# Optimization experiments

Hardware: AMD Instinct MI355X
Metric: run time of the kernel (lower is better)

## Reference

```python
import jax, jax.numpy as jnp
import numpy as np

H = 16          # heads_num
EPS_LN = 1e-6
EPS_RMS = 1e-6


def _layernorm(x):
    # elementwise_affine=False LayerNorm over last dim
    mu = jnp.mean(x, axis=-1, keepdims=True)
    var = jnp.mean(jnp.square(x - mu), axis=-1, keepdims=True)
    return (x - mu) * jax.lax.rsqrt(var + EPS_LN)


def _rmsnorm(x, w):
    # per-head RMSNorm over head_dim with affine weight
    ms = jnp.mean(jnp.square(x), axis=-1, keepdims=True)
    return x * jax.lax.rsqrt(ms + EPS_RMS) * w


def setup_inputs() -> dict:
    key = jax.random.key(0)
    ks = jax.random.split(key, 16)
    B, L, C = 2, 2048, 2048
    D = C // H
    Cm = 4 * C  # mlp hidden (mlp_width_ratio=4)
    s = 0.02
    return {
        "txt": jax.random.normal(ks[0], (B, L, C), jnp.float32),
        "vec_txt": jax.random.normal(ks[1], (B, C), jnp.float32),
        "mod_w": jax.random.normal(ks[2], (C, 6 * C), jnp.float32) * s,
        "mod_b": jnp.zeros((6 * C,), jnp.float32),
        "q_w": jax.random.normal(ks[3], (C, C), jnp.float32) * s,
        "k_w": jax.random.normal(ks[4], (C, C), jnp.float32) * s,
        "v_w": jax.random.normal(ks[5], (C, C), jnp.float32) * s,
        "qn_w": jnp.ones((D,), jnp.float32),
        "kn_w": jnp.ones((D,), jnp.float32),
        "proj_w": jax.random.normal(ks[6], (C, C), jnp.float32) * s,
        "fc1_w": jax.random.normal(ks[7], (C, Cm), jnp.float32) * s,
        "fc1_b": jnp.zeros((Cm,), jnp.float32),
        "fc2_w": jax.random.normal(ks[8], (Cm, C), jnp.float32) * s,
        "fc2_b": jnp.zeros((C,), jnp.float32),
    }


def _block(txt, vec_txt, mod_w, mod_b, q_w, k_w, v_w, qn_w, kn_w,
           proj_w, fc1_w, fc1_b, fc2_w, fc2_b):
    B, L, C = txt.shape
    D = C // H
    # ModulateDiT: Linear(silu(vec)) -> 6 chunks
    mod = jax.nn.silu(vec_txt) @ mod_w + mod_b                  # [B, 6C]
    sh1, sc1, g1, sh2, sc2, g2 = jnp.split(mod, 6, axis=-1)     # each [B, C]

    xm = _layernorm(txt) * (1.0 + sc1[:, None, :]) + sh1[:, None, :]
    q = (xm @ q_w).reshape(B, L, H, D)
    k = (xm @ k_w).reshape(B, L, H, D)
    v = (xm @ v_w).reshape(B, L, H, D)
    q = _rmsnorm(q, qn_w)
    k = _rmsnorm(k, kn_w)

    # causal scaled dot-product attention
    scores = jnp.einsum('blhd,bmhd->bhlm', q, k) / jnp.sqrt(jnp.float32(D))
    causal = jnp.tril(jnp.ones((L, L), bool))
    scores = jnp.where(causal[None, None], scores, jnp.finfo(scores.dtype).min)
    probs = jax.nn.softmax(scores, axis=-1)
    attn = jnp.einsum('bhlm,bmhd->blhd', probs, v).reshape(B, L, C)

    txt = txt + g1[:, None, :] * (attn @ proj_w)

    x2 = _layernorm(txt) * (1.0 + sc2[:, None, :]) + sh2[:, None, :]
    mlp = jax.nn.gelu(x2 @ fc1_w + fc1_b, approximate=True) @ fc2_w + fc2_b
    txt = txt + g2[:, None, :] * mlp
    return txt


def reference(txt, vec_txt, mod_w, mod_b, q_w, k_w, v_w, qn_w, kn_w,
              proj_w, fc1_w, fc1_b, fc2_w, fc2_b):
    return _block(txt, vec_txt, mod_w, mod_b, q_w, k_w, v_w, qn_w, kn_w,
                  proj_w, fc1_w, fc1_b, fc2_w, fc2_b)
```

## Files before the change

### kernel.cpp

```cpp
#include <hip/hip_runtime.h>
#include <math.h>

typedef unsigned short u16;
typedef unsigned int   u32;
typedef __attribute__((ext_vector_type(8))) short short8;
typedef __attribute__((ext_vector_type(4))) float f32x4;

#define H_   16
#define B_   2
#define L_   2048
#define C_   2048
#define D_   128
#define CM_  8192
#define SIXC_ (6*C_)
#define M_   (B_*L_)

__device__ __forceinline__ u16 f2bf(float f) {
  u32 u = __float_as_uint(f);
  u = (u + 0x7fffu + ((u >> 16) & 1u)) >> 16;
  return (u16)u;
}

__global__ __launch_bounds__(256)
void wt_transpose(const float* __restrict__ Wf, u16* __restrict__ Wt, int K, int N)
{
  __shared__ float tile[32][33];
  const int n0 = blockIdx.x * 32, k0 = blockIdx.y * 32;
  const int t = threadIdx.x;
  const int r = t >> 5, c = t & 31;
  #pragma unroll
  for (int i = 0; i < 4; i++)
    tile[i*8 + r][c] = Wf[(long)(k0 + i*8 + r)*N + n0 + c];
  __syncthreads();
  #pragma unroll
  for (int i = 0; i < 4; i++)
    Wt[(long)(n0 + i*8 + r)*K + k0 + c] = f2bf(tile[c][i*8 + r]);
}

__global__ __launch_bounds__(256)
void v_transpose(const float* __restrict__ vf, u16* __restrict__ vt)
{
  __shared__ float tile[32][33];
  const int l0 = blockIdx.x * 32, d0 = blockIdx.y * 32;
  const int bh = blockIdx.z;
  const int b = bh >> 4, h = bh & 15;
  const int t = threadIdx.x;
  const int r = t >> 5, c = t & 31;
  #pragma unroll
  for (int i = 0; i < 4; i++)
    tile[i*8 + r][c] = vf[(((long)b*L_ + l0 + i*8 + r)*H_ + h)*D_ + d0 + c];
  __syncthreads();
  #pragma unroll
  for (int i = 0; i < 4; i++)
    vt[((long)bh*D_ + d0 + i*8 + r)*L_ + l0 + c] = f2bf(tile[c][i*8 + r]);
}

__global__ __launch_bounds__(256)
void mod_init(const float* __restrict__ mb, float* __restrict__ mod)
{
  int i = blockIdx.x * 256 + threadIdx.x;
  mod[i] = mb[i % SIXC_];
}

__global__ __launch_bounds__(256)
void mod_accum(const float* __restrict__ vec, const float* __restrict__ mw,
               float* __restrict__ mod)
{
  const int j  = blockIdx.x * 256 + threadIdx.x;
  const int c0 = blockIdx.y * 128;
  const int b  = blockIdx.z;
  float s = 0.f;
  for (int c = c0; c < c0 + 128; c++) {
    float v  = vec[b*C_ + c];
    float sv = v / (1.0f + expf(-v));
    s += sv * mw[(long)c*SIXC_ + j];
  }
  atomicAdd(&mod[b*SIXC_ + j], s);
}

__global__ __launch_bounds__(256)
void ln_mod(const float* __restrict__ x, const float* __restrict__ mod,
            u16* __restrict__ out, int sh_off, int sc_off)
{
  const int row = blockIdx.x;
  const int b   = row >> 11;
  const int t   = threadIdx.x;
  const int l   = t & 63, w = t >> 6;
  const float* xr = x + (long)row * C_;
  float4 v0 = *(const float4*)(xr + t*8);
  float4 v1 = *(const float4*)(xr + t*8 + 4);
  float xs[8] = {v0.x, v0.y, v0.z, v0.w, v1.x, v1.y, v1.z, v1.w};
  float s = 0.f;
  #pragma unroll
  for (int i = 0; i < 8; i++) s += xs[i];
  #pragma unroll
  for (int o = 1; o < 64; o <<= 1) s += __shfl_xor(s, o, 64);
  __shared__ float r1[4], r2[4];
  if (l == 0) r1[w] = s;
  __syncthreads();
  float mu = (r1[0] + r1[1] + r1[2] + r1[3]) * (1.0f / C_);
  float vs = 0.f;
  #pragma unroll
  for (int i = 0; i < 8; i++) { float d = xs[i] - mu; vs += d*d; }
  #pragma unroll
  for (int o = 1; o < 64; o <<= 1) vs += __shfl_xor(vs, o, 64);
  if (l == 0) r2[w] = vs;
  __syncthreads();
  float var  = (r2[0] + r2[1] + r2[2] + r2[3]) * (1.0f / C_);
  float rstd = rsqrtf(var + 1e-6f);
  const float* shp = mod + b*SIXC_ + sh_off;
  const float* scp = mod + b*SIXC_ + sc_off;
  u16 o8[8];
  #pragma unroll
  for (int i = 0; i < 8; i++) {
    int col = t*8 + i;
    o8[i] = f2bf((xs[i] - mu)*rstd*(1.0f + scp[col]) + shp[col]);
  }
  *(short8*)(out + (long)row*C_ + t*8) = *(short8*)o8;
}

__global__ __launch_bounds__(256)
void rms_cast(const float* __restrict__ in, const float* __restrict__ w,
              u16* __restrict__ out)
{
  const int row = blockIdx.x;
  const int t   = threadIdx.x;
  const long base = (long)row*C_ + t*8;
  float4 v0 = *(const float4*)(in + base);
  float4 v1 = *(const float4*)(in + base + 4);
  float xs[8] = {v0.x, v0.y, v0.z, v0.w, v1.x, v1.y, v1.z, v1.w};
  float ss = 0.f;
  #pragma unroll
  for (int i = 0; i < 8; i++) ss += xs[i]*xs[i];
  #pragma unroll
  for (int o = 1; o < 16; o <<= 1) ss += __shfl_xor(ss, o, 64);
  float sc = rsqrtf(ss * (1.0f/D_) + 1e-6f);
  const int d0 = (t & 15) * 8;
  u16 o8[8];
  #pragma unroll
  for (int i = 0; i < 8; i++) o8[i] = f2bf(xs[i]*sc*w[d0 + i]);
  *(short8*)(out + base) = *(short8*)o8;
}

template<int MODE>
__global__ __launch_bounds__(256)
void gemm_bt(const u16* __restrict__ A, const u16* __restrict__ Bt,
             int N, int K,
             float* __restrict__ Cf, u16* __restrict__ Cb,
             const float* __restrict__ bias,
             const float* __restrict__ resid,
             const float* __restrict__ mod, int goff)
{
  __shared__ __attribute__((aligned(16))) u16 As[128*32];
  __shared__ __attribute__((aligned(16))) u16 Bs[128*32];
  const int tid = threadIdx.x;
  const int l   = tid & 63;
  const int llo = l & 15, lhi = l >> 4;
  const int w   = tid >> 6;
  const int m0 = blockIdx.y * 128, n0 = blockIdx.x * 128;
  const int wm = (w >> 1) * 64, wn = (w & 1) * 64;

  const u16* Ag = A  + (long)m0 * K;
  const u16* Bg = Bt + (long)n0 * K;

  const int srow0 = (w*2)*16 + (l >> 2);
  const int skoff = (l & 3) * 8;

  f32x4 acc[4][4];
  #pragma unroll
  for (int i = 0; i < 4; i++)
    #pragma unroll
    for (int j = 0; j < 4; j++) acc[i][j] = (f32x4){0.f, 0.f, 0.f, 0.f};

  for (int k0 = 0; k0 < K; k0 += 32) {
    __syncthreads();
    #pragma unroll
    for (int i = 0; i < 2; i++) {
      const u16* ga = Ag + (long)(srow0 + i*16)*K + k0 + skoff;
      const u16* gb = Bg + (long)(srow0 + i*16)*K + k0 + skoff;
      __builtin_amdgcn_global_load_lds(
          (const __attribute__((address_space(1))) void*)ga,
          (__attribute__((address_space(3))) void*)(As + (w*2 + i)*512), 16, 0, 0);
      __builtin_amdgcn_global_load_lds(
          (const __attribute__((address_space(1))) void*)gb,
          (__attribute__((address_space(3))) void*)(Bs + (w*2 + i)*512), 16, 0, 0);
    }
    __syncthreads();
    short8 a[4], b[4];
    #pragma unroll
    for (int f = 0; f < 4; f++) {
      a[f] = *(const short8*)&As[(wm + f*16 + llo)*32 + lhi*8];
      b[f] = *(const short8*)&Bs[(wn + f*16 + llo)*32 + lhi*8];
    }
    #pragma unroll
    for (int mf = 0; mf < 4; mf++)
      #pragma unroll
      for (int nf = 0; nf < 4; nf++)
        acc[mf][nf] = __builtin_amdgcn_mfma_f32_16x16x32_bf16(a[mf], b[nf], acc[mf][nf], 0, 0, 0);
  }

  #pragma unroll
  for (int mf = 0; mf < 4; mf++) {
    #pragma unroll
    for (int j = 0; j < 4; j++) {
      const int  r  = m0 + wm + mf*16 + lhi*4 + j;
      const long rb = (long)r * N;
      const int  bb = r >> 11;
      #pragma unroll
      for (int nf = 0; nf < 4; nf++) {
        const int col = n0 + wn + nf*16 + llo;
        float x = acc[mf][nf][j];
        if (MODE == 0) {
          Cf[rb + col] = x;
        } else if (MODE == 1) {
          x += bias[col];
          float g = 0.5f*x*(1.0f + tanhf(0.7978845608028654f*(x + 0.044715f*x*x*x)));
          Cb[rb + col] = f2bf(g);
        } else if (MODE == 2) {
          Cf[rb + col] = resid[rb + col] + mod[bb*SIXC_ + goff + col] * x;
        } else {
          Cf[rb + col] = resid[rb + col] + mod[bb*SIXC_ + goff + col] * (x + bias[col]);
        }
      }
    }
  }
}

__global__ __launch_bounds__(256)
void attn(const u16* __restrict__ qb, const u16* __restrict__ kb,
          const u16* __restrict__ vt, u16* __restrict__ out)
{
  const int w = threadIdx.x >> 6;
  const int l = threadIdx.x & 63;
  const int p  = blockIdx.x * 4 + w;
  const int bh = blockIdx.y;
  const int b = bh >> 4, h = bh & 15;
  const int llo = l & 15, lhi = l >> 4;

  __shared__ __attribute__((aligned(16))) u16 Plds[4][16*32];
  u16* Pl = &Plds[w][0];

  const u16* kbase = kb + ((long)b*L_*H_ + h)*D_;
  const u16* vbase = vt + (long)bh*D_*L_;
  const float scale = 0.08838834764831845f;

  #pragma unroll
  for (int pass = 0; pass < 2; pass++) {
    const int qt = pass ? (127 - p) : p;
    const int q0 = qt * 16;

    short8 qf[4];
    const u16* qrow = qb + (((long)b*L_ + q0 + llo)*H_ + h)*D_;
    #pragma unroll
    for (int dc = 0; dc < 4; dc++) qf[dc] = *(const short8*)(qrow + dc*32 + lhi*8);

    f32x4 o[8];
    #pragma unroll
    for (int f = 0; f < 8; f++) o[f] = (f32x4){0.f, 0.f, 0.f, 0.f};
    float mreg = -1e30f, lsum = 0.f;

    const int ntiles = (q0 + 16 + 31) >> 5;

    for (int kt = 0; kt < ntiles; kt++) {
      const int kv0 = kt * 32;
      f32x4 st[2];
      st[0] = (f32x4){0.f,0.f,0.f,0.f};
      st[1] = (f32x4){0.f,0.f,0.f,0.f};
      #pragma unroll
      for (int mf = 0; mf < 2; mf++) {
        const u16* krow = kbase + (long)(kv0 + mf*16 + llo)*(H_*D_);
        #pragma unroll
        for (int dc = 0; dc < 4; dc++) {
          short8 kfr = *(const short8*)(krow + dc*32 + lhi*8);
          st[mf] = __builtin_amdgcn_mfma_f32_16x16x32_bf16(kfr, qf[dc], st[mf], 0, 0, 0);
        }
      }
      const int qcol = q0 + llo;
      float sv[8];
      float tmax = -1e30f;
      #pragma unroll
      for (int mf = 0; mf < 2; mf++)
        #pragma unroll
        for (int j = 0; j < 4; j++) {
          int key = kv0 + mf*16 + lhi*4 + j;
          float x = st[mf][j] * scale;
          x = (key > qcol) ? -1e30f : x;
          sv[mf*4 + j] = x;
          tmax = fmaxf(tmax, x);
        }
      tmax = fmaxf(tmax, __shfl_xor(tmax, 16, 64));
      tmax = fmaxf(tmax, __shfl_xor(tmax, 32, 64));
      float mnew  = fmaxf(mreg, tmax);
      float alpha = __expf(mreg - mnew);
      float psum = 0.f;
      u16 pb[8];
      #pragma unroll
      for (int i = 0; i < 8; i++) {
        float pp = __expf(sv[i] - mnew);
        psum += pp;
        pb[i] = f2bf(pp);
      }
      psum += __shfl_xor(psum, 16, 64);
      psum += __shfl_xor(psum, 32, 64);
      lsum = lsum*alpha + psum;
      mreg = mnew;
      #pragma unroll
      for (int j = 0; j < 4; j++) {
        float aj = __shfl(alpha, lhi*4 + j, 64);
        #pragma unroll
        for (int f = 0; f < 8; f++) o[f][j] *= aj;
      }
      #pragma unroll
      for (int mf = 0; mf < 2; mf++) {
        u32 w0 = (u32)pb[mf*4+0] | ((u32)pb[mf*4+1] << 16);
        u32 w1 = (u32)pb[mf*4+2] | ((u32)pb[mf*4+3] << 16);
        *(u32*)&Pl[llo*32 + mf*16 + lhi*4]     = w0;
        *(u32*)&Pl[llo*32 + mf*16 + lhi*4 + 2] = w1;
      }
      asm volatile("s_waitcnt lgkmcnt(0)" ::: "memory");
      short8 pf = *(const short8*)&Pl[llo*32 + lhi*8];
      #pragma unroll
      for (int f = 0; f < 8; f++) {
        short8 vfr = *(const short8*)(vbase + (long)(f*16 + llo)*L_ + kv0 + lhi*8);
        o[f] = __builtin_amdgcn_mfma_f32_16x16x32_bf16(pf, vfr, o[f], 0, 0, 0);
      }
      asm volatile("s_waitcnt lgkmcnt(0)" ::: "memory");
    }

    #pragma unroll
    for (int j = 0; j < 4; j++) {
      float lq  = __shfl(lsum, lhi*4 + j, 64);
      float inv = 1.0f / lq;
      const int qr = q0 + lhi*4 + j;
      u16* orow = out + ((long)b*L_ + qr)*C_ + h*D_;
      #pragma unroll
      for (int f = 0; f < 8; f++)
        orow[f*16 + llo] = f2bf(o[f][j] * inv);
    }
  }
}

extern "C" void kernel_launch(void* const* d_in, const int* in_sizes, int n_in,
                              void* d_out, int out_size, void* d_ws, size_t ws_size,
                              hipStream_t stream)
{
  const float* txt    = (const float*)d_in[0];
  const float* vec    = (const float*)d_in[1];
  const float* mod_w  = (const float*)d_in[2];
  const float* mod_b  = (const float*)d_in[3];
  const float* q_w    = (const float*)d_in[4];
  const float* k_w    = (const float*)d_in[5];
  const float* v_w    = (const float*)d_in[6];
  const float* qn_w   = (const float*)d_in[7];
  const float* kn_w   = (const float*)d_in[8];
  const float* proj_w = (const float*)d_in[9];
  const float* fc1_w  = (const float*)d_in[10];
  const float* fc1_b  = (const float*)d_in[11];
  const float* fc2_w  = (const float*)d_in[12];
  const float* fc2_b  = (const float*)d_in[13];
  float* out = (float*)d_out;

  char* ws = (char*)d_ws;
  size_t off = 0;
  auto alloc = [&](size_t bytes) {
    size_t r = off; off += (bytes + 255) & ~(size_t)255; return r;
  };
  float* mod  = (float*)(ws + alloc((size_t)B_*SIXC_*4));
  u16*  qwt   = (u16*)(ws + alloc((size_t)C_*C_*2));
  u16*  kwt   = (u16*)(ws + alloc((size_t)C_*C_*2));
  u16*  vwt   = (u16*)(ws + alloc((size_t)C_*C_*2));
  u16*  pwt   = (u16*)(ws + alloc((size_t)C_*C_*2));
  u16*  f1wt  = (u16*)(ws + alloc((size_t)C_*CM_*2));
  u16*  f2wt  = (u16*)(ws + alloc((size_t)C_*CM_*2));
  u16*  xm    = (u16*)(ws + alloc((size_t)M_*C_*2));
  float* qf   = (float*)(ws + alloc((size_t)M_*C_*4));
  float* kf   = (float*)(ws + alloc((size_t)M_*C_*4));
  float* vf   = (float*)(ws + alloc((size_t)M_*C_*4));
  u16*  qbb   = (u16*)(ws + alloc((size_t)M_*C_*2));
  u16*  kbb   = (u16*)(ws + alloc((size_t)M_*C_*2));
  u16*  vtt   = (u16*)(ws + alloc((size_t)M_*C_*2));
  u16*   h1     = (u16*)kf;
  float* txt2   = qf;
  u16*   x2m    = qbb;
  u16*   attn_o = xm;

  wt_transpose<<<dim3(C_/32,  C_/32 ), 256, 0, stream>>>(q_w,    qwt,  C_,  C_);
  wt_transpose<<<dim3(C_/32,  C_/32 ), 256, 0, stream>>>(k_w,    kwt,  C_,  C_);
  wt_transpose<<<dim3(C_/32,  C_/32 ), 256, 0, stream>>>(v_w,    vwt,  C_,  C_);
  wt_transpose<<<dim3(C_/32,  C_/32 ), 256, 0, stream>>>(proj_w, pwt,  C_,  C_);
  wt_transpose<<<dim3(CM_/32, C_/32 ), 256, 0, stream>>>(fc1_w,  f1wt, C_,  CM_);
  wt_transpose<<<dim3(C_/32,  CM_/32), 256, 0, stream>>>(fc2_w,  f2wt, CM_, C_);

  mod_init <<<dim3(B_*SIXC_/256), 256, 0, stream>>>(mod_b, mod);
  mod_accum<<<dim3(SIXC_/256, C_/128, B_), 256, 0, stream>>>(vec, mod_w, mod);

  ln_mod<<<dim3(M_), 256, 0, stream>>>(txt, mod, xm, 0, C_);

  gemm_bt<0><<<dim3(C_/128, M_/128), 256, 0, stream>>>(xm, qwt, C_, C_, qf, nullptr, nullptr, nullptr, nullptr, 0);
  gemm_bt<0><<<dim3(C_/128, M_/128), 256, 0, stream>>>(xm, kwt, C_, C_, kf, nullptr, nullptr, nullptr, nullptr, 0);
  gemm_bt<0><<<dim3(C_/128, M_/128), 256, 0, stream>>>(xm, vwt, C_, C_, vf, nullptr, nullptr, nullptr, nullptr, 0);

  rms_cast<<<dim3(M_), 256, 0, stream>>>(qf, qn_w, qbb);
  rms_cast<<<dim3(M_), 256, 0, stream>>>(kf, kn_w, kbb);
  v_transpose<<<dim3(L_/32, D_/32, B_*H_), 256, 0, stream>>>(vf, vtt);

  attn<<<dim3(L_/16/4/2, B_*H_), 256, 0, stream>>>(qbb, kbb, vtt, attn_o);

  gemm_bt<2><<<dim3(C_/128, M_/128), 256, 0, stream>>>(attn_o, pwt, C_, C_, txt2, nullptr, nullptr, txt, mod, 2*C_);

  ln_mod<<<dim3(M_), 256, 0, stream>>>(txt2, mod, x2m, 3*C_, 4*C_);

  gemm_bt<1><<<dim3(CM_/128, M_/128), 256, 0, stream>>>(x2m, f1wt, CM_, C_, nullptr, h1, fc1_b, nullptr, nullptr, 0);

  gemm_bt<3><<<dim3(C_/128, M_/128), 256, 0, stream>>>(h1, f2wt, C_, CM_, out, nullptr, fc2_b, txt2, mod, 5*C_);
}
```

Before: 1.322 ms.

## Pre-swizzle Q/K/V into MFMA fragment order and give each attention wave one tile

After: 1.251 ms. 1.06x faster.

```diff
diff --git a/kernel.cpp b/kernel.cpp
--- a/kernel.cpp
+++ b/kernel.cpp
@@ -38,7 +38,7 @@
 }
 
 __global__ __launch_bounds__(256)
-void v_transpose(const float* __restrict__ vf, u16* __restrict__ vt)
+void v_transpose(const float* __restrict__ vf, u16* __restrict__ vp)
 {
   __shared__ float tile[32][33];
   const int l0 = blockIdx.x * 32, d0 = blockIdx.y * 32;
@@ -50,9 +50,18 @@
   for (int i = 0; i < 4; i++)
     tile[i*8 + r][c] = vf[(((long)b*L_ + l0 + i*8 + r)*H_ + h)*D_ + d0 + c];
   __syncthreads();
-  #pragma unroll
-  for (int i = 0; i < 4; i++)
-    vt[((long)bh*D_ + d0 + i*8 + r)*L_ + l0 + c] = f2bf(tile[c][i*8 + r]);
+  if (t < 128) {
+    const int dl  = t >> 2;
+    const int oct = t & 3;
+    const int d   = d0 + dl;
+    const int f   = d >> 4, vllo = d & 15;
+    const int kt  = l0 >> 5;
+    u16 o8[8];
+    #pragma unroll
+    for (int e = 0; e < 8; e++) o8[e] = f2bf(tile[oct*8 + e][dl]);
+    u16* dst = vp + (((((long)bh*64 + kt)*8 + f)*4 + oct)*16 + vllo)*8;
+    *(short8*)dst = *(short8*)o8;
+  }
 }
 
 __global__ __launch_bounds__(256)
@@ -120,11 +129,15 @@
 }
 
 __global__ __launch_bounds__(256)
-void rms_cast(const float* __restrict__ in, const float* __restrict__ w,
-              u16* __restrict__ out)
+void rms_swz(const float* __restrict__ in, const float* __restrict__ w,
+             u16* __restrict__ out)
 {
   const int row = blockIdx.x;
+  const int b = row >> 11, lseq = row & 2047;
+  const int g = lseq >> 4, llo = lseq & 15;
   const int t   = threadIdx.x;
+  const int h   = t >> 4, c16 = t & 15;
+  const int dc  = c16 >> 2, lhi = c16 & 3;
   const long base = (long)row*C_ + t*8;
   float4 v0 = *(const float4*)(in + base);
   float4 v1 = *(const float4*)(in + base + 4);
@@ -135,11 +148,12 @@
   #pragma unroll
   for (int o = 1; o < 16; o <<= 1) ss += __shfl_xor(ss, o, 64);
   float sc = rsqrtf(ss * (1.0f/D_) + 1e-6f);
-  const int d0 = (t & 15) * 8;
+  const int d0 = c16 * 8;
   u16 o8[8];
   #pragma unroll
   for (int i = 0; i < 8; i++) o8[i] = f2bf(xs[i]*sc*w[d0 + i]);
-  *(short8*)(out + base) = *(short8*)o8;
+  u16* dst = out + (((((long)(b*H_ + h)*128 + g)*4 + dc)*4 + lhi)*16 + llo)*8;
+  *(short8*)dst = *(short8*)o8;
 }
 
 template<int MODE>
@@ -226,117 +240,119 @@
   }
 }
 
-__global__ __launch_bounds__(256)
-void attn(const u16* __restrict__ qb, const u16* __restrict__ kb,
-          const u16* __restrict__ vt, u16* __restrict__ out)
+__global__ __launch_bounds__(256, 4)
+void attn(const u16* __restrict__ qs, const u16* __restrict__ ks,
+          const u16* __restrict__ vp, u16* __restrict__ out)
 {
   const int w = threadIdx.x >> 6;
   const int l = threadIdx.x & 63;
-  const int p  = blockIdx.x * 4 + w;
+  const int qt = 127 - (blockIdx.x * 4 + w);
   const int bh = blockIdx.y;
-  const int b = bh >> 4, h = bh & 15;
+  const int b = bh >> 4;
+  const int h = bh & 15;
   const int llo = l & 15, lhi = l >> 4;
 
   __shared__ __attribute__((aligned(16))) u16 Plds[4][16*32];
   u16* Pl = &Plds[w][0];
 
-  const u16* kbase = kb + ((long)b*L_*H_ + h)*D_;
-  const u16* vbase = vt + (long)bh*D_*L_;
+  const u16* qbase = qs + ((long)bh*128 + qt)*2048;
+  const u16* kbase = ks + (long)bh*262144;
+  const u16* vbase = vp + (long)bh*262144;
   const float scale = 0.08838834764831845f;
 
-  #pragma unroll
-  for (int pass = 0; pass < 2; pass++) {
-    const int qt = pass ? (127 - p) : p;
-    const int q0 = qt * 16;
-
-    short8 qf[4];
-    const u16* qrow = qb + (((long)b*L_ + q0 + llo)*H_ + h)*D_;
-    #pragma unroll
-    for (int dc = 0; dc < 4; dc++) qf[dc] = *(const short8*)(qrow + dc*32 + lhi*8);
-
-    f32x4 o[8];
-    #pragma unroll
-    for (int f = 0; f < 8; f++) o[f] = (f32x4){0.f, 0.f, 0.f, 0.f};
-    float mreg = -1e30f, lsum = 0.f;
-
-    const int ntiles = (q0 + 16 + 31) >> 5;
-
-    for (int kt = 0; kt < ntiles; kt++) {
-      const int kv0 = kt * 32;
-      f32x4 st[2];
-      st[0] = (f32x4){0.f,0.f,0.f,0.f};
-      st[1] = (f32x4){0.f,0.f,0.f,0.f};
+  short8 qf[4];
+  #pragma unroll
+  for (int dc = 0; dc < 4; dc++)
+    qf[dc] = *(const short8*)(qbase + dc*512 + l*8);
+
+  f32x4 o[8];
+  #pragma unroll
+  for (int f = 0; f < 8; f++) o[f] = (f32x4){0.f, 0.f, 0.f, 0.f};
+  float mreg = -1e30f, lsum = 0.f;
+
+  const int ntiles = (qt + 2) >> 1;
+  const int qcol = qt*16 + llo;
+
+  for (int kt = 0; kt < ntiles; kt++) {
+    const int kv0 = kt * 32;
+    const u16* ktb = kbase + (long)kt*4096;
+    const u16* vtb = vbase + (long)kt*4096;
+
+    f32x4 st[2];
+    st[0] = (f32x4){0.f,0.f,0.f,0.f};
+    st[1] = (f32x4){0.f,0.f,0.f,0.f};
+    #pragma unroll
+    for (int mf = 0; mf < 2; mf++) {
       #pragma unroll
-      for (int mf = 0; mf < 2; mf++) {
-        const u16* krow = kbase + (long)(kv0 + mf*16 + llo)*(H_*D_);
-        #pragma unroll
-        for (int dc = 0; dc < 4; dc++) {
-          short8 kfr = *(const short8*)(krow + dc*32 + lhi*8);
-          st[mf] = __builtin_amdgcn_mfma_f32_16x16x32_bf16(kfr, qf[dc], st[mf], 0, 0, 0);
-        }
+      for (int dc = 0; dc < 4; dc++) {
+        short8 kfr = *(const short8*)(ktb + mf*2048 + dc*512 + l*8);
+        st[mf] = __builtin_amdgcn_mfma_f32_16x16x32_bf16(kfr, qf[dc], st[mf], 0, 0, 0);
       }
-      const int qcol = q0 + llo;
-      float sv[8];
-      float tmax = -1e30f;
-      #pragma unroll
-      for (int mf = 0; mf < 2; mf++)
-        #pragma unroll
-        for (int j = 0; j < 4; j++) {
-          int key = kv0 + mf*16 + lhi*4 + j;
-          float x = st[mf][j] * scale;
-          x = (key > qcol) ? -1e30f : x;
-          sv[mf*4 + j] = x;
-          tmax = fmaxf(tmax, x);
-        }
-      tmax = fmaxf(tmax, __shfl_xor(tmax, 16, 64));
-      tmax = fmaxf(tmax, __shfl_xor(tmax, 32, 64));
-      float mnew  = fmaxf(mreg, tmax);
-      float alpha = __expf(mreg - mnew);
-      float psum = 0.f;
-      u16 pb[8];
-      #pragma unroll
-      for (int i = 0; i < 8; i++) {
-        float pp = __expf(sv[i] - mnew);
-        psum += pp;
-        pb[i] = f2bf(pp);
-      }
-      psum += __shfl_xor(psum, 16, 64);
-      psum += __shfl_xor(psum, 32, 64);
-      lsum = lsum*alpha + psum;
-      mreg = mnew;
+    }
+
+    short8 vfr[8];
+    #pragma unroll
+    for (int f = 0; f < 8; f++)
+      vfr[f] = *(const short8*)(vtb + f*512 + l*8);
+
+    float sv[8];
+    float tmax = -1e30f;
+    #pragma unroll
+    for (int mf = 0; mf < 2; mf++)
       #pragma unroll
       for (int j = 0; j < 4; j++) {
-        float aj = __shfl(alpha, lhi*4 + j, 64);
-        #pragma unroll
-        for (int f = 0; f < 8; f++) o[f][j] *= aj;
+        int key = kv0 + mf*16 + lhi*4 + j;
+        float x = st[mf][j] * scale;
+        x = (key > qcol) ? -1e30f : x;
+        sv[mf*4 + j] = x;
+        tmax = fmaxf(tmax, x);
       }
+    tmax = fmaxf(tmax, __shfl_xor(tmax, 16, 64));
+    tmax = fmaxf(tmax, __shfl_xor(tmax, 32, 64));
+    float mnew  = fmaxf(mreg, tmax);
+    float alpha = __expf(mreg - mnew);
+    float psum = 0.f;
+    u16 pb[8];
+    #pragma unroll
+    for (int i = 0; i < 8; i++) {
+      float pp = __expf(sv[i] - mnew);
+      psum += pp;
+      pb[i] = f2bf(pp);
+    }
+    psum += __shfl_xor(psum, 16, 64);
+    psum += __shfl_xor(psum, 32, 64);
+    lsum = lsum*alpha + psum;
+    mreg = mnew;
+    #pragma unroll
+    for (int j = 0; j < 4; j++) {
+      float aj = __shfl(alpha, lhi*4 + j, 64);
       #pragma unroll
-      for (int mf = 0; mf < 2; mf++) {
-        u32 w0 = (u32)pb[mf*4+0] | ((u32)pb[mf*4+1] << 16);
-        u32 w1 = (u32)pb[mf*4+2] | ((u32)pb[mf*4+3] << 16);
-        *(u32*)&Pl[llo*32 + mf*16 + lhi*4]     = w0;
-        *(u32*)&Pl[llo*32 + mf*16 + lhi*4 + 2] = w1;
-      }
-      asm volatile("s_waitcnt lgkmcnt(0)" ::: "memory");
-      short8 pf = *(const short8*)&Pl[llo*32 + lhi*8];
-      #pragma unroll
-      for (int f = 0; f < 8; f++) {
-        short8 vfr = *(const short8*)(vbase + (long)(f*16 + llo)*L_ + kv0 + lhi*8);
-        o[f] = __builtin_amdgcn_mfma_f32_16x16x32_bf16(pf, vfr, o[f], 0, 0, 0);
-      }
-      asm volatile("s_waitcnt lgkmcnt(0)" ::: "memory");
-    }
-
-    #pragma unroll
-    for (int j = 0; j < 4; j++) {
-      float lq  = __shfl(lsum, lhi*4 + j, 64);
-      float inv = 1.0f / lq;
-      const int qr = q0 + lhi*4 + j;
-      u16* orow = out + ((long)b*L_ + qr)*C_ + h*D_;
-      #pragma unroll
-      for (int f = 0; f < 8; f++)
-        orow[f*16 + llo] = f2bf(o[f][j] * inv);
-    }
+      for (int f = 0; f < 8; f++) o[f][j] *= aj;
+    }
+    #pragma unroll
+    for (int mf = 0; mf < 2; mf++) {
+      u32 w0 = (u32)pb[mf*4+0] | ((u32)pb[mf*4+1] << 16);
+      u32 w1 = (u32)pb[mf*4+2] | ((u32)pb[mf*4+3] << 16);
+      *(u32*)&Pl[llo*32 + mf*16 + lhi*4]     = w0;
+      *(u32*)&Pl[llo*32 + mf*16 + lhi*4 + 2] = w1;
+    }
+    asm volatile("s_waitcnt lgkmcnt(0)" ::: "memory");
+    short8 pf = *(const short8*)&Pl[llo*32 + lhi*8];
+    #pragma unroll
+    for (int f = 0; f < 8; f++)
+      o[f] = __builtin_amdgcn_mfma_f32_16x16x32_bf16(pf, vfr[f], o[f], 0, 0, 0);
+    asm volatile("s_waitcnt lgkmcnt(0)" ::: "memory");
+  }
+
+  #pragma unroll
+  for (int j = 0; j < 4; j++) {
+    float lq  = __shfl(lsum, lhi*4 + j, 64);
+    float inv = 1.0f / lq;
+    const int qr = qt*16 + lhi*4 + j;
+    u16* orow = out + ((long)b*L_ + qr)*C_ + h*D_;
+    #pragma unroll
+    for (int f = 0; f < 8; f++)
+      orow[f*16 + llo] = f2bf(o[f][j] * inv);
   }
 }
 
@@ -400,11 +416,11 @@
   gemm_bt<0><<<dim3(C_/128, M_/128), 256, 0, stream>>>(xm, kwt, C_, C_, kf, nullptr, nullptr, nullptr, nullptr, 0);
   gemm_bt<0><<<dim3(C_/128, M_/128), 256, 0, stream>>>(xm, vwt, C_, C_, vf, nullptr, nullptr, nullptr, nullptr, 0);
 
-  rms_cast<<<dim3(M_), 256, 0, stream>>>(qf, qn_w, qbb);
-  rms_cast<<<dim3(M_), 256, 0, stream>>>(kf, kn_w, kbb);
+  rms_swz<<<dim3(M_), 256, 0, stream>>>(qf, qn_w, qbb);
+  rms_swz<<<dim3(M_), 256, 0, stream>>>(kf, kn_w, kbb);
   v_transpose<<<dim3(L_/32, D_/32, B_*H_), 256, 0, stream>>>(vf, vtt);
 
-  attn<<<dim3(L_/16/4/2, B_*H_), 256, 0, stream>>>(qbb, kbb, vtt, attn_o);
+  attn<<<dim3(L_/16/4, B_*H_), 256, 0, stream>>>(qbb, kbb, vtt, attn_o);
 
   gemm_bt<2><<<dim3(C_/128, M_/128), 256, 0, stream>>>(attn_o, pwt, C_, C_, txt2, nullptr, nullptr, txt, mod, 2*C_);
 
```
